# Performance work log

Hardware: AMD Instinct MI355X
Metric: run time of the kernel (lower is better)

## Reference

```python
import jax, jax.numpy as jnp
import numpy as np

# dims
B, N, M, R = 2, 16384, 512, 8      # batch, points, modes (slices), register tokens
D = 384                             # q_dim == kv_dim
H, DH = 8, 48                       # heads, dim_heads
P = 3                               # phys_dim
NF = DH // (2 * P)                  # rope freqs per physical axis (8)
FH = 1024                           # gated FFN hidden
L = 2                               # num_interleaved_layers
MINLF, MAXLF = -5.0, 3.0
EPS_LN = 1e-5
EPS_NORM = 1e-8


def _ln(x, g, b):
    m = jnp.mean(x, -1, keepdims=True)
    v = jnp.var(x, -1, keepdims=True)
    return (x - m) * jax.lax.rsqrt(v + EPS_LN) * g + b


def _rope_cs(coords):
    # coords: (B, S, P) -> cos/sin of shape (B, S, DH//2)
    freqs = jnp.exp(jnp.linspace(MINLF, MAXLF, NF))
    ang = (coords[..., :, None] * freqs).reshape(coords.shape[:-1] + (P * NF,))
    return jnp.cos(ang), jnp.sin(ang)


def _apply_rope(t, c, s):
    # t: (B, S, H, DH); c,s: (B, S, DH//2)
    tp = t.reshape(t.shape[:-1] + (DH // 2, 2))
    t0, t1 = tp[..., 0], tp[..., 1]
    c = c[:, :, None, :]
    s = s[:, :, None, :]
    r = jnp.stack([t0 * c - t1 * s, t0 * s + t1 * c], axis=-1)
    return r.reshape(t.shape)


def _mha(qin, kin, vin, xq, xk, wq, bq, wk, bk, wv, bv, wo, bo):
    Bq, Sq, _ = qin.shape
    Sk = kin.shape[1]
    q = (qin @ wq + bq).reshape(Bq, Sq, H, DH)
    k = (kin @ wk + bk).reshape(Bq, Sk, H, DH)
    v = (vin @ wv + bv).reshape(Bq, Sk, H, DH)
    cq, sq = _rope_cs(xq)
    ck, sk = _rope_cs(xk)
    q = _apply_rope(q, cq, sq)
    k = _apply_rope(k, ck, sk)
    scores = jnp.einsum('bqhd,bkhd->bhqk', q, k) / np.sqrt(DH).astype(np.float32)
    a = jax.nn.softmax(scores, axis=-1)
    o = jnp.einsum('bhqk,bkhd->bqhd', a, v).reshape(Bq, Sq, H * DH)
    return o @ wo + bo


def _subgen(feat, w, b):
    # Transolver slice generator: softmax over modes per point; mass == 1.
    tf = jax.nn.softmax(feat @ w + b, axis=-1)          # (B, S, M) trial_func
    tt = jnp.swapaxes(tf, 1, 2)                          # (B, M, S) trial_in_t
    inv = 1.0 / (jnp.sum(tf, axis=1) + EPS_NORM)         # (B, M) inv_trial_norm
    return tf, tt, inv[..., None]


def setup_inputs() -> dict:
    key = jax.random.key(0)
    ks = iter(jax.random.split(key, 64))
    nrm = lambda shape: jax.random.normal(next(ks), shape, dtype=jnp.float32)
    w = lambda shape: nrm(shape) * 0.02
    inp = {}
    inp['qx'] = nrm((B, N, D))
    inp['kvx'] = nrm((B, N, D))
    inp['x'] = jax.random.uniform(next(ks), (B, N, P), dtype=jnp.float32)
    inp['reg_tok_qx'] = nrm((B, R, D))
    inp['reg_tok_x'] = jax.random.uniform(next(ks), (B, R, P), dtype=jnp.float32)
    inp['subq_w'] = w((D, M)); inp['subq_b'] = jnp.zeros((M,))
    inp['subkv_w'] = w((D, M)); inp['subkv_b'] = jnp.zeros((M,))
    inp['nq_g'] = jnp.ones((D,)); inp['nq_b'] = jnp.zeros((D,))
    inp['nkv_g'] = jnp.ones((D,)); inp['nkv_b'] = jnp.zeros((D,))
    inp['a0_wq'] = w((D, H * DH)); inp['a0_bq'] = jnp.zeros((H * DH,))
    inp['a0_wk'] = w((D, H * DH)); inp['a0_bk'] = jnp.zeros((H * DH,))
    inp['a0_wv'] = w((D, H * DH)); inp['a0_bv'] = jnp.zeros((H * DH,))
    inp['a0_wo'] = w((H * DH, D)); inp['a0_bo'] = jnp.zeros((D,))
    inp['out_g'] = jnp.ones((D,)); inp['out_b'] = jnp.zeros((D,))
    inp['L_wq'] = w((L, D, H * DH)); inp['L_bq'] = jnp.zeros((L, H * DH))
    inp['L_wk'] = w((L, D, H * DH)); inp['L_bk'] = jnp.zeros((L, H * DH))
    inp['L_wv'] = w((L, D, H * DH)); inp['L_bv'] = jnp.zeros((L, H * DH))
    inp['L_wo'] = w((L, H * DH, D)); inp['L_bo'] = jnp.zeros((L, D))
    inp['L_ang'] = jnp.ones((L, D)); inp['L_anb'] = jnp.zeros((L, D))
    inp['L_fng'] = jnp.ones((L, D)); inp['L_fnb'] = jnp.zeros((L, D))
    inp['L_wg'] = w((L, D, FH)); inp['L_bg'] = jnp.zeros((L, FH))
    inp['L_wu'] = w((L, D, FH)); inp['L_bu'] = jnp.zeros((L, FH))
    inp['L_wd'] = w((L, FH, D)); inp['L_bd'] = jnp.zeros((L, D))
    return inp


def reference(qx, kvx, x, reg_tok_qx, reg_tok_x,
              subq_w, subq_b, subkv_w, subkv_b,
              nq_g, nq_b, nkv_g, nkv_b,
              a0_wq, a0_bq, a0_wk, a0_bk, a0_wv, a0_bv, a0_wo, a0_bo,
              out_g, out_b,
              L_wq, L_bq, L_wk, L_bk, L_wv, L_bv, L_wo, L_bo,
              L_ang, L_anb, L_fng, L_fnb,
              L_wg, L_bg, L_wu, L_bu, L_wd, L_bd):
    tfq, ttq, invq = _subgen(qx, subq_w, subq_b)
    _, ttkv, invkv = _subgen(kvx, subkv_w, subkv_b)
    qx_proj = jnp.matmul(ttq, qx) * invq          # (B, M, D)
    kvx_proj = jnp.matmul(ttkv, kvx) * invkv      # (B, M, D)
    xq_proj = jnp.matmul(ttq, x) * invq           # (B, M, P)
    xk_proj = jnp.matmul(ttkv, x) * invkv         # (B, M, P)
    q_full = jnp.concatenate([qx_proj, reg_tok_qx], axis=1)   # (B, M+R, D)
    xq_full = jnp.concatenate([xq_proj, reg_tok_x], axis=1)   # (B, M+R, P)
    q = _ln(q_full, nq_g, nq_b)
    kv = _ln(kvx_proj, nkv_g, nkv_b)
    y = _mha(q, kv, kv, xq_full, xk_proj,
             a0_wq, a0_bq, a0_wk, a0_bk, a0_wv, a0_bv, a0_wo, a0_bo) + q_full
    for i in range(L):
        h = _ln(y, L_fng[i], L_fnb[i])
        h = (jax.nn.silu(h @ L_wg[i] + L_bg[i]) * (h @ L_wu[i] + L_bu[i])) @ L_wd[i] + L_bd[i]
        y = h + y
        qn = _ln(y, L_ang[i], L_anb[i])
        y = _mha(qn, kv, kv, xq_full, xk_proj,
                 L_wq[i], L_bq[i], L_wk[i], L_bk[i], L_wv[i], L_bv[i], L_wo[i], L_bo[i]) + y
    y = _ln(y, out_g, out_b)
    y_proj = y[:, :M, :]
    reg_token = y[:, M:, :]
    y_recon = jnp.matmul(tfq, y_proj)             # (B, N, D)
    return (y_recon, reg_token)
```

## Files before the change

kernel.cpp:

```cpp
#include <hip/hip_runtime.h>


typedef __attribute__((ext_vector_type(8))) short short8;
typedef __attribute__((ext_vector_type(4))) float floatx4;

__device__ __forceinline__ float b2f(short s) {
    unsigned u = ((unsigned)(unsigned short)s) << 16;
    return __builtin_bit_cast(float, u);
}
__device__ __forceinline__ short f2b(float f) {
    unsigned u = __builtin_bit_cast(unsigned, f);
    unsigned r = (u + 0x7fffu + ((u >> 16) & 1u)) >> 16;
    return (short)r;
}

__device__ __forceinline__ void gload_lds16(const short* g, short* l) {
    __builtin_amdgcn_global_load_lds(
        (const __attribute__((address_space(1))) void*)(g),
        (__attribute__((address_space(3))) void*)(l), 16, 0, 0);
}

__global__ __launch_bounds__(256) void cvt_bf16_2(
    const float* __restrict__ srcA, const float* __restrict__ srcB,
    short* __restrict__ dstA, short* __restrict__ dstB, long n)
{
    const float* src = blockIdx.y ? srcB : srcA;
    short* dst = blockIdx.y ? dstB : dstA;
    long i = ((long)blockIdx.x * 256 + threadIdx.x) * 4;
    if (i + 4 <= n) {
        float4 v = *(const float4*)(src + i);
        short o[4] = {f2b(v.x), f2b(v.y), f2b(v.z), f2b(v.w)};
        *(short4*)(dst + i) = *(short4*)o;
    } else {
        for (long j = i; j < n; j++) dst[j] = f2b(src[j]);
    }
}

template <int EPI, bool SPLITK>
__global__ __launch_bounds__(256) void gemm_nt(
    const short* __restrict__ A, int lda, long sAb, long sAh,
    const short* __restrict__ Bm, int ldb, long sBb, long sBh,
    void* Cp, int ldc, long sCb, long sCh,
    const float* __restrict__ bias, int biasRow, int bzs,
    const float* aux, int ldaux,
    int Mrows, int Ncols, int Kdim, int nb, int KC)
{
    int z = blockIdx.z;
    int b = z % nb;
    int rest = z / nb;
    long aoff = (long)b * sAb, boff = (long)b * sBb;
    long coff = (long)b * sCb + (long)rest * sCh;
    int k_begin = 0, kEnd = Kdim;
    if (SPLITK) {
        k_begin = rest * KC;
        int ke = k_begin + KC;
        kEnd = ke < Kdim ? ke : Kdim;
    } else {
        aoff += (long)rest * sAh;
        boff += (long)rest * sBh;
    }
    if (bias) bias += (long)rest * bzs;
    const short* Ap = A + aoff;
    const short* Bp = Bm + boff;

    int row0 = blockIdx.x * 128, col0 = blockIdx.y * 128;
    __shared__ __align__(16) short As[3 * 128 * 32];
    __shared__ __align__(16) short Bs[3 * 128 * 32];
    int tid = threadIdx.x, lane = tid & 63, wv = tid >> 6;
    int wr = (wv >> 1) * 64, wc = (wv & 1) * 64;
    int lr = lane & 15, lq = lane >> 4;

    const bool fullMN = (row0 + 128 <= Mrows) && (col0 + 128 <= Ncols);
    const int kLen = kEnd - k_begin;
    const int nSteps = (kLen + 31) >> 5;
    const bool useRing = fullMN && ((kLen & 31) == 0);

    const int frow = (wv << 5) + (lane >> 2);
    const int fk = (lane & 3) << 3;
    const short* gA0 = Ap + (long)(row0 + frow) * lda + fk;
    const short* gA1 = gA0 + 16 * (long)lda;
    const short* gB0 = Bp + (long)(col0 + frow) * ldb + fk;
    const short* gB1 = gB0 + 16 * (long)ldb;
    short* lA0 = As + (wv << 10);
    short* lA1 = lA0 + 512;
    short* lB0 = Bs + (wv << 10);
    short* lB1 = lB0 + 512;

    auto stageFast = [&](int slot, int k0) {
        int bo = slot << 12;
        gload_lds16(gA0 + k0, lA0 + bo);
        gload_lds16(gA1 + k0, lA1 + bo);
        gload_lds16(gB0 + k0, lB0 + bo);
        gload_lds16(gB1 + k0, lB1 + bo);
    };
    auto stageAny = [&](int slot, int k0) {
        if (fullMN && (k0 + 32 <= kEnd)) {
            stageFast(slot, k0);
        } else {
            short* Ab = As + (slot << 12);
            short* Bb = Bs + (slot << 12);
#pragma unroll
            for (int io = 0; io < 2; io++) {
                int sid = tid * 2 + io;
                int r = sid >> 2, sg = sid & 3;
                int gk = k0 + sg * 8;
                short8 va, vb;
#pragma unroll
                for (int j = 0; j < 8; j++) { va[j] = 0; vb[j] = 0; }
                int gra = row0 + r, grb = col0 + r;
                if (gra < Mrows) {
                    const short* p = Ap + (long)gra * lda + gk;
                    if (gk + 8 <= kEnd) va = *(const short8*)p;
                    else { for (int j = 0; j < 8; j++) if (gk + j < kEnd) va[j] = p[j]; }
                }
                if (grb < Ncols) {
                    const short* p = Bp + (long)grb * ldb + gk;
                    if (gk + 8 <= kEnd) vb = *(const short8*)p;
                    else { for (int j = 0; j < 8; j++) if (gk + j < kEnd) vb[j] = p[j]; }
                }
                *(short8*)&Ab[r * 32 + sg * 8] = va;
                *(short8*)&Bb[r * 32 + sg * 8] = vb;
            }
        }
    };

    floatx4 acc[4][4];
#pragma unroll
    for (int i = 0; i < 4; i++)
#pragma unroll
        for (int j = 0; j < 4; j++)
#pragma unroll
            for (int e = 0; e < 4; e++) acc[i][j][e] = 0.f;

    auto compute = [&](int slot) {
        const int co = slot << 12;
        short8 af[4], bfv[4];
#pragma unroll
        for (int mt = 0; mt < 4; mt++)
            af[mt] = *(const short8*)&As[co + (wr + mt * 16 + lr) * 32 + lq * 8];
#pragma unroll
        for (int nt = 0; nt < 4; nt++)
            bfv[nt] = *(const short8*)&Bs[co + (wc + nt * 16 + lr) * 32 + lq * 8];
#pragma unroll
        for (int mt = 0; mt < 4; mt++)
#pragma unroll
            for (int nt = 0; nt < 4; nt++)
                acc[mt][nt] = __builtin_amdgcn_mfma_f32_16x16x32_bf16(
                    af[mt], bfv[nt], acc[mt][nt], 0, 0, 0);
    };

    if (useRing) {
        stageFast(0, k_begin);
        if (nSteps > 1) stageFast(1, k_begin + 32);
        int slotCur = 0, slotPre = 2;
        for (int s = 0; s < nSteps; s++) {
            if (s < nSteps - 1)
                asm volatile("s_waitcnt vmcnt(4)" ::: "memory");
            else
                asm volatile("s_waitcnt vmcnt(0)" ::: "memory");
            __builtin_amdgcn_s_barrier();
            __builtin_amdgcn_sched_barrier(0);
            if (s + 2 < nSteps) stageFast(slotPre, k_begin + (s + 2) * 32);
            compute(slotCur);
            slotCur = (slotCur == 2) ? 0 : slotCur + 1;
            slotPre = (slotPre == 2) ? 0 : slotPre + 1;
        }
    } else {
        stageAny(0, k_begin);
        __syncthreads();
        for (int s = 0; s < nSteps; s++) {
            const int cur = s & 1;
            if (s + 1 < nSteps) stageAny(cur ^ 1, k_begin + (s + 1) * 32);
            compute(cur);
            __syncthreads();
        }
    }

    if (EPI == 5) {
        const float ropeScale = __builtin_bit_cast(float, KC);
        const float* cosT = aux;
        const float* sinT = aux + ldaux;
#pragma unroll
        for (int mt = 0; mt < 4; mt++) {
#pragma unroll
            for (int nt = 0; nt < 4; nt++) {
                int gcol = col0 + wc + nt * 16 + lr;
#pragma unroll
                for (int r = 0; r < 4; r++) {
                    int grow = row0 + wr + mt * 16 + lq * 4 + r;
                    float v = acc[mt][nt][r] + bias[gcol];
                    float partner = __shfl_xor(v, 1, 64);
                    if (fullMN || (grow < Mrows && gcol < Ncols)) {
                        int pi = (gcol >> 1) % 24;
                        float cc = cosT[(long)grow * 24 + pi];
                        float ss = sinT[(long)grow * 24 + pi];
                        float o = (gcol & 1) ? (partner * ss + v * cc)
                                             : (v * cc - partner * ss);
                        ((short*)Cp)[coff + (long)grow * ldc + gcol] =
                            f2b(o * ropeScale);
                    }
                }
            }
        }
    } else if (EPI == 6) {
#pragma unroll
        for (int mt = 0; mt < 4; mt++) {
#pragma unroll
            for (int nt = 0; nt < 4; nt++) {
                int gcol = col0 + wc + nt * 16 + lr;
#pragma unroll
                for (int r = 0; r < 4; r++) {
                    int grow = row0 + wr + mt * 16 + lq * 4 + r;
                    float v = acc[mt][nt][r] + bias[gcol];
                    float partner = __shfl_xor(v, 1, 64);
                    if (((gcol & 1) == 0) && (fullMN || grow < Mrows)) {
                        float s = v / (1.f + __expf(-v));
                        ((short*)Cp)[coff + (long)grow * ldc + (gcol >> 1)] =
                            f2b(s * partner);
                    }
                }
            }
        }
    } else if (fullMN) {
#pragma unroll
        for (int mt = 0; mt < 4; mt++) {
#pragma unroll
            for (int nt = 0; nt < 4; nt++) {
                int gcol = col0 + wc + nt * 16 + lr;
#pragma unroll
                for (int r = 0; r < 4; r++) {
                    int grow = row0 + wr + mt * 16 + lq * 4 + r;
                    float v = acc[mt][nt][r];
                    if (bias) v += bias[biasRow ? grow : gcol];
                    long idx = coff + (long)grow * ldc + gcol;
                    if (EPI == 0) {
                        ((float*)Cp)[idx] = v;
                    } else if (EPI == 1) {
                        ((short*)Cp)[idx] = f2b(v);
                    } else {
                        float rr = aux[(long)grow * ldaux + gcol];
                        ((float*)Cp)[idx] = v + rr;
                    }
                }
            }
        }
    } else {
#pragma unroll
        for (int mt = 0; mt < 4; mt++) {
#pragma unroll
            for (int nt = 0; nt < 4; nt++) {
                int gcol = col0 + wc + nt * 16 + lr;
#pragma unroll
                for (int r = 0; r < 4; r++) {
                    int grow = row0 + wr + mt * 16 + lq * 4 + r;
                    if (grow < Mrows && gcol < Ncols) {
                        float v = acc[mt][nt][r];
                        if (bias) v += bias[biasRow ? grow : gcol];
                        long idx = coff + (long)grow * ldc + gcol;
                        if (EPI == 0) {
                            ((float*)Cp)[idx] = v;
                        } else if (EPI == 1) {
                            ((short*)Cp)[idx] = f2b(v);
                        } else {
                            float rr = aux[(long)grow * ldaux + gcol];
                            ((float*)Cp)[idx] = v + rr;
                        }
                    }
                }
            }
        }
    }
}

__global__ __launch_bounds__(64) void attn_fused(
    const short* __restrict__ Q, const short* __restrict__ K,
    const short* __restrict__ V, short* __restrict__ O)
{
    int tile = blockIdx.x;
    int b = blockIdx.y, h = blockIdx.z;
    int lane = threadIdx.x;
    int lr = lane & 15, lq = lane >> 4;
    int q0 = tile * 16;

    const short* Qb = Q + (long)b * 199680 + h * 48;
    const short* Kb = K + (long)b * 196608 + h * 48;
    const short* Vb = V + (long)b * 196608 + (long)h * 48 * 512;
    short* Ob = O + (long)b * 199680 + h * 48;

    __shared__ __align__(16) short Plds[16 * 512];
    char* pb = (char*)Plds;

    short8 aq0, aq1;
    {
        int qr = q0 + lr; if (qr > 519) qr = 519;
        const short* qp = Qb + (long)qr * 384;
        aq0 = *(const short8*)(qp + lq * 8);
        short8 z;
#pragma unroll
        for (int j = 0; j < 8; j++) z[j] = 0;
        aq1 = (lq < 2) ? *(const short8*)(qp + 32 + lq * 8) : z;
    }

    floatx4 s[32];
#pragma unroll
    for (int nt = 0; nt < 32; nt++)
#pragma unroll
        for (int e = 0; e < 4; e++) s[nt][e] = 0.f;
#pragma unroll
    for (int nt = 0; nt < 32; nt++) {
        const short* kp = Kb + (long)(nt * 16 + lr) * 384;
        short8 b0 = *(const short8*)(kp + lq * 8);
        short8 b1 = *(const short8*)(kp + 32 + lq * 8);
        s[nt] = __builtin_amdgcn_mfma_f32_16x16x32_bf16(aq0, b0, s[nt], 0, 0, 0);
        s[nt] = __builtin_amdgcn_mfma_f32_16x16x32_bf16(aq1, b1, s[nt], 0, 0, 0);
    }

    float mx[4], sum[4], inv[4];
#pragma unroll
    for (int r = 0; r < 4; r++) mx[r] = -1e30f;
#pragma unroll
    for (int nt = 0; nt < 32; nt++)
#pragma unroll
        for (int r = 0; r < 4; r++) mx[r] = fmaxf(mx[r], s[nt][r]);
#pragma unroll
    for (int o = 8; o; o >>= 1)
#pragma unroll
        for (int r = 0; r < 4; r++) mx[r] = fmaxf(mx[r], __shfl_xor(mx[r], o, 64));
#pragma unroll
    for (int r = 0; r < 4; r++) sum[r] = 0.f;
#pragma unroll
    for (int nt = 0; nt < 32; nt++)
#pragma unroll
        for (int r = 0; r < 4; r++) {
            float e = __expf(s[nt][r] - mx[r]);
            s[nt][r] = e;
            sum[r] += e;
        }
#pragma unroll
    for (int o = 8; o; o >>= 1)
#pragma unroll
        for (int r = 0; r < 4; r++) sum[r] += __shfl_xor(sum[r], o, 64);
#pragma unroll
    for (int r = 0; r < 4; r++) inv[r] = 1.0f / sum[r];

#pragma unroll
    for (int nt = 0; nt < 32; nt++)
#pragma unroll
        for (int r = 0; r < 4; r++) {
            int row = lq * 4 + r, col = nt * 16 + lr;
            int byo = ((row * 512 + col) * 2) ^ ((row & 7) << 4);
            *(short*)(pb + byo) = f2b(s[nt][r] * inv[r]);
        }

    floatx4 o2[3];
#pragma unroll
    for (int nt = 0; nt < 3; nt++)
#pragma unroll
        for (int e = 0; e < 4; e++) o2[nt][e] = 0.f;
#pragma unroll
    for (int ks = 0; ks < 16; ks++) {
        int byo = ((lr * 512 + ks * 32 + lq * 8) * 2) ^ ((lr & 7) << 4);
        short8 ap = *(const short8*)(pb + byo);
#pragma unroll
        for (int nt = 0; nt < 3; nt++) {
            short8 bv = *(const short8*)(Vb + (long)(nt * 16 + lr) * 512 +
                                         ks * 32 + lq * 8);
            o2[nt] = __builtin_amdgcn_mfma_f32_16x16x32_bf16(ap, bv, o2[nt], 0, 0, 0);
        }
    }
#pragma unroll
    for (int nt = 0; nt < 3; nt++)
#pragma unroll
        for (int r = 0; r < 4; r++) {
            int q = q0 + lq * 4 + r;
            if (q < 520)
                Ob[(long)q * 384 + nt * 16 + lr] = f2b(o2[nt][r]);
        }
}

__global__ __launch_bounds__(256) void softmax_rows(
    const short* __restrict__ src, short* __restrict__ dstN,
    short* __restrict__ dstT, int rowsPerBatch)
{
    int n0 = blockIdx.x * 32;
    __shared__ __align__(16) short tile[32 * 512];
    int tid = threadIdx.x;
    const short8* gsrc = (const short8*)(src + (long)n0 * 512);
    short8* t8 = (short8*)tile;
#pragma unroll
    for (int i = 0; i < 8; i++) t8[tid + i * 256] = gsrc[tid + i * 256];
    __syncthreads();
    int wv = tid >> 6, lane = tid & 63;
#pragma unroll
    for (int rr = 0; rr < 8; rr++) {
        int r = wv * 8 + rr;
        short8 s = *(const short8*)&tile[r * 512 + lane * 8];
        float v[8];
        float mx = -1e30f;
#pragma unroll
        for (int j = 0; j < 8; j++) { v[j] = b2f(s[j]); mx = fmaxf(mx, v[j]); }
#pragma unroll
        for (int o = 32; o; o >>= 1) mx = fmaxf(mx, __shfl_xor(mx, o, 64));
        float sum = 0.f;
#pragma unroll
        for (int j = 0; j < 8; j++) { v[j] = __expf(v[j] - mx); sum += v[j]; }
#pragma unroll
        for (int o = 32; o; o >>= 1) sum += __shfl_xor(sum, o, 64);
        float inv = 1.0f / sum;
        short8 o8;
#pragma unroll
        for (int j = 0; j < 8; j++) o8[j] = f2b(v[j] * inv);
        *(short8*)&tile[r * 512 + lane * 8] = o8;
        if (dstN) *(short8*)(dstN + (long)(n0 + r) * 512 + lane * 8) = o8;
    }
    if (!dstT) return;
    __syncthreads();
    int b = n0 / rowsPerBatch;
    int nn0 = n0 % rowsPerBatch;
#pragma unroll
    for (int rep = 0; rep < 2; rep++) {
        int m = tid + rep * 256;
        short tmp[32];
#pragma unroll
        for (int i = 0; i < 32; i++) tmp[i] = tile[i * 512 + m];
        short* dst = dstT + ((long)b * 512 + m) * rowsPerBatch + nn0;
#pragma unroll
        for (int i = 0; i < 4; i++) *(short8*)(dst + i * 8) = *(const short8*)&tmp[i * 8];
    }
}

__global__ __launch_bounds__(256) void build_augT(
    const short* __restrict__ src, const float* __restrict__ xin,
    short* __restrict__ augT)
{
    int n0 = blockIdx.x * 32, jb = blockIdx.y, b = blockIdx.z;
    int t = threadIdx.x;
    if (jb == 12) {
        if (t < 128) {
            int jj = t >> 5, i = t & 31;
            float val = (jj < 3) ? xin[((long)b * 16384 + n0 + i) * 3 + jj] : 1.0f;
            augT[((long)(b * 512 + 384 + jj)) * 16384 + n0 + i] = f2b(val);
        }
        return;
    }
    __shared__ short tl[32][33];
    int j0 = jb * 32;
#pragma unroll
    for (int rep = 0; rep < 4; rep++) {
        int sid = t + rep * 256;
        int i = sid >> 5, j = sid & 31;
        tl[i][j] = src[((long)b * 16384 + n0 + i) * 384 + j0 + j];
    }
    __syncthreads();
#pragma unroll
    for (int rep = 0; rep < 4; rep++) {
        int sid = t + rep * 256;
        int j = sid >> 5, i = sid & 31;
        augT[((long)(b * 512 + j0 + j)) * 16384 + n0 + i] = tl[i][j];
    }
}

template <bool ISQ>
__global__ __launch_bounds__(256) void prep_kernel(
    const float* __restrict__ parts, const float* __restrict__ regqx,
    const float* __restrict__ regx, const float* __restrict__ gam,
    const float* __restrict__ bet, float* __restrict__ qfull,
    short* __restrict__ lnout, float* __restrict__ cb, float* __restrict__ sb,
    int Srows)
{
    int m = blockIdx.x, b = blockIdx.y, t = threadIdx.x;
    __shared__ float sh[388];
    __shared__ float r1[256], r2[256];
    bool isReg = ISQ && (m >= 512);
    if (isReg) {
        int rr = m - 512;
        for (int c = t; c < 384; c += 256) sh[c] = regqx[((long)b * 8 + rr) * 384 + c];
        if (t < 3) sh[384 + t] = regx[((long)b * 8 + rr) * 3 + t];
    } else {
        for (int c = t; c < 388; c += 256) {
            float s = 0.f;
#pragma unroll
            for (int sp = 0; sp < 16; sp++)
                s += parts[(((long)(sp * 2 + b)) * 512 + m) * 512 + c];
            sh[c] = s;
        }
    }
    __syncthreads();
    float inv = isReg ? 1.0f : 1.0f / (sh[387] + 1e-8f);
    float ls = 0.f, lq = 0.f;
    for (int c = t; c < 384; c += 256) {
        float v = sh[c] * inv;
        ls += v; lq += v * v;
    }
    r1[t] = ls; r2[t] = lq;
    __syncthreads();
    for (int o = 128; o; o >>= 1) {
        if (t < o) { r1[t] += r1[t + o]; r2[t] += r2[t + o]; }
        __syncthreads();
    }
    float mean = r1[0] * (1.f / 384.f);
    float var = r2[0] * (1.f / 384.f) - mean * mean;
    float rs = rsqrtf(var + 1e-5f);
    long row = (long)b * Srows + m;
    for (int c = t; c < 384; c += 256) {
        float v = sh[c] * inv;
        if (ISQ) qfull[row * 384 + c] = v;
        lnout[row * 384 + c] = f2b((v - mean) * rs * gam[c] + bet[c]);
    }
    if (t < 24) {
        int p = t >> 3, f = t & 7;
        float coord = sh[384 + p] * inv;
        float ang = coord * __expf(-5.0f + (float)f * (8.0f / 7.0f));
        cb[row * 24 + t] = cosf(ang);
        sb[row * 24 + t] = sinf(ang);
    }
}

struct TEntry { const float* src; short* dst; int rows, cols, cs, co; };
struct TTable { TEntry e[20]; int cnt; };

__global__ __launch_bounds__(256) void transpose_many(
    TTable tab, const float* __restrict__ a0bk, const float* __restrict__ Lbk,
    const float* __restrict__ a0bv, const float* __restrict__ Lbv,
    const float* __restrict__ Lbg, const float* __restrict__ Lbu,
    float* __restrict__ bkAll, float* __restrict__ bvAll,
    float* __restrict__ bgu)
{
    int id = blockIdx.z;
    int t = threadIdx.x;
    if (id >= tab.cnt) {
        if (blockIdx.x == 0 && blockIdx.y == 0) {
            for (int i = t; i < 1152; i += 256) {
                int l = i / 384, j = i % 384;
                bkAll[i] = l ? Lbk[(l - 1) * 384 + j] : a0bk[j];
                bvAll[i] = l ? Lbv[(l - 1) * 384 + j] : a0bv[j];
            }
            for (int i = t; i < 4096; i += 256) {
                int l = i >> 11, j = i & 2047;
                bgu[i] = (j & 1) ? Lbu[l * 1024 + (j >> 1)]
                                 : Lbg[l * 1024 + (j >> 1)];
            }
        }
        return;
    }
    TEntry E = tab.e[id];
    int r0 = blockIdx.y * 32, c0 = blockIdx.x * 32;
    if (r0 >= E.rows || c0 >= E.cols) return;
    __shared__ short tl[32][33];
#pragma unroll
    for (int rep = 0; rep < 4; rep++) {
        int sid = t + rep * 256;
        int i = sid >> 5, j = sid & 31;
        int r = r0 + i, c = c0 + j;
        tl[i][j] = (r < E.rows && c < E.cols) ? f2b(E.src[(long)r * E.cols + c])
                                              : (short)0;
    }
    __syncthreads();
#pragma unroll
    for (int rep = 0; rep < 4; rep++) {
        int sid = t + rep * 256;
        int j = sid >> 5, i = sid & 31;
        int c = c0 + j, r = r0 + i;
        if (c < E.cols && r < E.rows)
            E.dst[((long)c * E.cs + E.co) * E.rows + r] = tl[i][j];
    }
}

__global__ __launch_bounds__(256) void ln_kernel(
    const float* __restrict__ in, const float* __restrict__ gam,
    const float* __restrict__ bet, short* __restrict__ out)
{
    long row = blockIdx.x;
    int t = threadIdx.x;
    const float* xr = in + row * 384;
    float v0 = xr[t];
    float v1 = (t < 128) ? xr[t + 256] : 0.f;
    __shared__ float r1[256], r2[256];
    r1[t] = v0 + v1; r2[t] = v0 * v0 + v1 * v1;
    __syncthreads();
    for (int o = 128; o; o >>= 1) {
        if (t < o) { r1[t] += r1[t + o]; r2[t] += r2[t + o]; }
        __syncthreads();
    }
    float mean = r1[0] * (1.f / 384.f);
    float var = r2[0] * (1.f / 384.f) - mean * mean;
    float rs = rsqrtf(var + 1e-5f);
    out[row * 384 + t] = f2b((v0 - mean) * rs * gam[t] + bet[t]);
    if (t < 128)
        out[row * 384 + t + 256] =
            f2b((v1 - mean) * rs * gam[t + 256] + bet[t + 256]);
}

__global__ __launch_bounds__(256) void outln_kernel(
    const float* __restrict__ in, const float* __restrict__ gam,
    const float* __restrict__ bet, short* __restrict__ yln,
    short* __restrict__ ylnT, float* __restrict__ regout)
{
    int m = blockIdx.x, b = blockIdx.y, t = threadIdx.x;
    long row = (long)b * 520 + m;
    const float* xr = in + row * 384;
    float v0 = xr[t];
    float v1 = (t < 128) ? xr[t + 256] : 0.f;
    __shared__ float r1[256], r2[256];
    r1[t] = v0 + v1; r2[t] = v0 * v0 + v1 * v1;
    __syncthreads();
    for (int o = 128; o; o >>= 1) {
        if (t < o) { r1[t] += r1[t + o]; r2[t] += r2[t + o]; }
        __syncthreads();
    }
    float mean = r1[0] * (1.f / 384.f);
    float var = r2[0] * (1.f / 384.f) - mean * mean;
    float rs = rsqrtf(var + 1e-5f);
    float o0 = (v0 - mean) * rs * gam[t] + bet[t];
    float o1 = (t < 128) ? (v1 - mean) * rs * gam[t + 256] + bet[t + 256] : 0.f;
    if (m < 512) {
        short s0 = f2b(o0);
        yln[((long)b * 512 + m) * 384 + t] = s0;
        ylnT[((long)b * 384 + t) * 512 + m] = s0;
        if (t < 128) {
            short s1 = f2b(o1);
            yln[((long)b * 512 + m) * 384 + t + 256] = s1;
            ylnT[((long)b * 384 + t + 256) * 512 + m] = s1;
        }
    } else {
        float* dst = regout + ((long)b * 8 + (m - 512)) * 384;
        dst[t] = o0;
        if (t < 128) dst[t + 256] = o1;
    }
}

__device__ __forceinline__ int chk3(float v, float lo, float hi) {
    if (!(v == v) || fabsf(v) > 3e38f) return 1;
    if (v < lo || v > hi) return 2;
    return 0;
}

__global__ __launch_bounds__(256) void probe_stages(
    const float* __restrict__ nqg, const float* __restrict__ qx,
    const short* __restrict__ subqT, const short* __restrict__ tfq,
    const float* __restrict__ qfull, const short* __restrict__ qln,
    const short* __restrict__ kvln, const float* __restrict__ cq,
    const short* __restrict__ Kr, const short* __restrict__ Vt,
    const short* __restrict__ Oc, const short* __restrict__ hg,
    const float* __restrict__ y, const short* __restrict__ ylnT,
    const float* __restrict__ dout, int* __restrict__ diag)
{
    int t = threadIdx.x;
    int task = blockIdx.x;
    __shared__ int sNaN, sRange, sPl;
    if (t == 0) { sNaN = 0; sRange = 0; sPl = 0; }
    __syncthreads();

    auto scanB = [&](const short* p, long n, float lo, float hi) {
        long stride = n / 2048; if (stride < 1) stride = 1;
        for (int j = 0; j < 8; j++) {
            long i = ((long)(t * 8 + j)) * stride;
            if (i >= n) break;
            int c = chk3(b2f(p[i]), lo, hi);
            if (c == 1) atomicOr(&sNaN, 1);
            else if (c == 2) atomicOr(&sRange, 1);
        }
    };
    auto scanF = [&](const float* p, long n, float lo, float hi) {
        long stride = n / 2048; if (stride < 1) stride = 1;
        for (int j = 0; j < 8; j++) {
            long i = ((long)(t * 8 + j)) * stride;
            if (i >= n) break;
            int c = chk3(p[i], lo, hi);
            if (c == 1) atomicOr(&sNaN, 1);
            else if (c == 2) atomicOr(&sRange, 1);
        }
    };

    int res = 0;
    if (task == 0) {
        int d1;
        {
            bool f32ones = true;
            for (int i = 0; i < 8; i++) if (nqg[i] != 1.0f) f32ones = false;
            d1 = f32ones ? 0 : 1;
        }
        int d2;
        {
            int plaus = 0;
            for (int i = 0; i < 64; i++) {
                float v = qx[i];
                float a = fabsf(v);
                if (v == v && a > 1e-4f && a < 16.f) plaus++;
            }
            d2 = (plaus >= 56) ? 0 : 1;
        }
        if (t == 0) diag[2] = d1 * 3 + d2;
        return;
    } else if (task == 1) {
        long n = 196608L;
        long stride = n / 2048; if (stride < 1) stride = 1;
        for (int j = 0; j < 8; j++) {
            long i = ((long)(t * 8 + j)) * stride;
            if (i >= n) break;
            float v = b2f(subqT[i]);
            float a = fabsf(v);
            if (!(v == v)) atomicOr(&sNaN, 1);
            else if (a >= 1e-7f && a <= 2.f) atomicAdd(&sPl, 1);
        }
        __syncthreads();
        res = sNaN ? 1 : ((sPl < 1228) ? 2 : 0);
        if (t == 0) diag[2 + 1] = res;
        return;
    }
    switch (task) {
        case 2: scanB(tfq, 16777216L, -1e-4f, 1.0001f); break;
        case 3: scanF(qfull, 399360L, -1e3f, 1e3f); break;
        case 4: scanB(qln, 399360L, -100.f, 100.f); break;
        case 5: scanB(kvln, 393216L, -100.f, 100.f); break;
        case 6: scanF(cq, 24960L, -1.0001f, 1.0001f); break;
        case 7: scanB(Kr, 399360L, -1e3f, 1e3f); break;
        case 8: scanB(Vt, 1179648L, -1e3f, 1e3f); break;
        case 9: scanB(Oc, 399360L, -1e3f, 1e3f); break;
        case 10: scanB(hg, 1064960L, -1e4f, 1e4f); break;
        case 11: scanF(y, 399360L, -1e5f, 1e5f); break;
        case 12: scanB(ylnT, 393216L, -100.f, 100.f); break;
        case 13: scanF(dout, 12589056L, -1e3f, 1e3f); break;
        default: break;
    }
    __syncthreads();
    res = sNaN ? 1 : (sRange ? 2 : 0);
    if (t == 0) diag[2 + task] = res;
}

__global__ void probe_combine(int* __restrict__ diag, unsigned wsMB)
{
    int firstBad = 0, kind = 0;
    for (int idx = 1; idx <= 13; idx++) {
        int r = diag[2 + idx];
        if (r != 0 && firstBad == 0) { firstBad = idx; kind = (r == 2) ? 1 : 0; }
    }
    int dd = diag[2];
    int wb;
    if (wsMB < 32) wb = 0; else if (wsMB < 48) wb = 1;
    else if (wsMB < 64) wb = 2; else if (wsMB < 80) wb = 3;
    else if (wsMB < 96) wb = 4; else if (wsMB < 100) wb = 5;
    else if (wsMB < 112) wb = 6; else if (wsMB < 128) wb = 7;
    else if (wsMB < 160) wb = 8; else if (wsMB < 224) wb = 9;
    else if (wsMB < 512) wb = 10; else wb = 11;

    int code = firstBad + 14 * (kind + 2 * (wb + 12 * dd));
    diag[0] = code;
    diag[1] = (firstBad == 0 && dd == 0) ? 1 : 0;
}

__global__ __launch_bounds__(256) void fill_out(float* __restrict__ out,
                                                const int* __restrict__ diag,
                                                long n)
{
    if (diag[1]) return;
    int code = diag[0];
    long i0 = ((long)blockIdx.x * 256 + threadIdx.x) * 8;
#pragma unroll
    for (int j = 0; j < 8; j++)
        if (i0 + j < n) out[i0 + j] = 0.f;
    if (i0 == 0)
        out[1] = ldexpf(1.0f + (float)(code & 255) * (1.0f / 256.0f),
                        (code >> 8) + 14);
}

#define LAUNCH_GEMM(EPI, SPLIT, GX, GY, GZ, A, LDA, SAB, SAH, B_, LDB, SBB,   \
                    SBH, C_, LDC, SCB, SCH, BIAS, BROW, BZS, AUX, LDAUX, M_,  \
                    N_, K_, NB, KC)                                           \
    gemm_nt<EPI, SPLIT><<<dim3(GX, GY, GZ), 256, 0, stream>>>(                \
        (const short*)(A), LDA, SAB, SAH, (const short*)(B_), LDB, SBB, SBH,  \
        (void*)(C_), LDC, SCB, SCH, (const float*)(BIAS), BROW, BZS,          \
        (const float*)(AUX), LDAUX, M_, N_, K_, NB, KC)

extern "C" void kernel_launch(void* const* d_in, const int* in_sizes, int n_in,
                              void* d_out, int out_size, void* d_ws,
                              size_t ws_size, hipStream_t stream)
{
    (void)in_sizes; (void)n_in; (void)out_size;
    const float* qx    = (const float*)d_in[0];
    const float* kvx   = (const float*)d_in[1];
    const float* xin   = (const float*)d_in[2];
    const float* regqx = (const float*)d_in[3];
    const float* regx  = (const float*)d_in[4];
    const float* subq_b  = (const float*)d_in[6];
    const float* subkv_b = (const float*)d_in[8];
    const float* nq_g = (const float*)d_in[9];
    const float* nq_b = (const float*)d_in[10];
    const float* nkv_g = (const float*)d_in[11];
    const float* nkv_b = (const float*)d_in[12];
    const float* a0_bq = (const float*)d_in[14];
    const float* a0_bk = (const float*)d_in[16];
    const float* a0_bv = (const float*)d_in[18];
    const float* a0_bo = (const float*)d_in[20];
    const float* out_g = (const float*)d_in[21];
    const float* out_b = (const float*)d_in[22];
    const float* L_bq = (const float*)d_in[24];
    const float* L_bk = (const float*)d_in[26];
    const float* L_bv = (const float*)d_in[28];
    const float* L_bo = (const float*)d_in[30];
    const float* L_ang = (const float*)d_in[31];
    const float* L_anb = (const float*)d_in[32];
    const float* L_fng = (const float*)d_in[33];
    const float* L_fnb = (const float*)d_in[34];
    const float* L_bg = (const float*)d_in[36];
    const float* L_bu = (const float*)d_in[38];
    const float* L_bd = (const float*)d_in[40];

    char* W = (char*)d_ws;
    short* qxb   = (short*)(W + 0L);
    short* kvxb  = (short*)(W + 25165824L);
    short* tfT   = (short*)(W + 50331648L);
    short* tfq   = (short*)(W + 83886080L);
    short* aug   = (short*)(W + 117440512L);
    short* Wt    = (short*)(W + 167772160L);
    float* qfull = (float*)(W + 176816128L);
    short* qln   = (short*)(W + 178413568L);
    short* kvln  = (short*)(W + 179212288L);
    float* cq    = (float*)(W + 179998720L);
    float* sq    = (float*)(W + 180098560L);
    float* ck    = (float*)(W + 180198400L);
    float* sk    = (float*)(W + 180296704L);
    float* y     = (float*)(W + 180395008L);
    short* hln   = (short*)(W + 181992448L);
    short* ylnT  = (short*)(W + 182791168L);
    short* VtAll = (short*)(W + 209136640L);
    short* Oc    = (short*)(W + 213396480L);
    float* bkAll = (float*)(W + 214195200L);
    float* bvAll = (float*)(W + 214200320L);
    float* bgu   = (float*)(W + 214205440L);
    short* Qr    = (short*)(W + 215792640L);
    short* hg    = (short*)(W + 218164224L);
    int*   diag  = (int*)(W + 220294144L);
    float* parts = (float*)(W + 220298240L);
    short* KrAll = tfT;

    short* subqT  = Wt + 0L;
    short* subkvT = Wt + 196608L;
    auto QW  = [&](int l) { return Wt + 393216L  + (long)l * 147456L; };
    auto KW  = [&](int l) { return Wt + 835584L  + (long)l * 147456L; };
    auto VW  = [&](int l) { return Wt + 1277952L + (long)l * 147456L; };
    auto OW  = [&](int l) { return Wt + 1720320L + (long)l * 147456L; };
    auto GUW = [&](int l) { return Wt + 2162688L + (long)l * 786432L; };
    auto DW  = [&](int l) { return Wt + 3735552L + (long)l * 393216L; };

    auto fbits = [](float f) {
        union { float f; int i; } u; u.f = f; return u.i;
    };

    cvt_bf16_2<<<dim3(12288, 2), 256, 0, stream>>>(qx, kvx, qxb, kvxb,
                                                   12582912L);

    TTable tt;
    int ti = 0;
    auto addT = [&](const void* s, short* dst, int r, int c, int cs, int co) {
        tt.e[ti].src = (const float*)s; tt.e[ti].dst = dst;
        tt.e[ti].rows = r; tt.e[ti].cols = c;
        tt.e[ti].cs = cs; tt.e[ti].co = co; ti++;
    };
    addT(d_in[5], subqT, 384, 512, 1, 0);
    addT(d_in[7], subkvT, 384, 512, 1, 0);
    addT(d_in[13], QW(0), 384, 384, 1, 0);
    addT(d_in[15], KW(0), 384, 384, 1, 0);
    addT(d_in[17], VW(0), 384, 384, 1, 0);
    addT(d_in[19], OW(0), 384, 384, 1, 0);
    for (int l = 0; l < 2; l++) {
        addT((const float*)d_in[23] + (long)l * 147456, QW(l + 1), 384, 384, 1, 0);
        addT((const float*)d_in[25] + (long)l * 147456, KW(l + 1), 384, 384, 1, 0);
        addT((const float*)d_in[27] + (long)l * 147456, VW(l + 1), 384, 384, 1, 0);
        addT((const float*)d_in[29] + (long)l * 147456, OW(l + 1), 384, 384, 1, 0);
        addT((const float*)d_in[35] + (long)l * 393216, GUW(l), 384, 1024, 2, 0);
        addT((const float*)d_in[37] + (long)l * 393216, GUW(l), 384, 1024, 2, 1);
        addT((const float*)d_in[39] + (long)l * 393216, DW(l), 1024, 384, 1, 0);
    }
    tt.cnt = ti;
    transpose_many<<<dim3(32, 32, 21), 256, 0, stream>>>(
        tt, a0_bk, L_bk, a0_bv, L_bv, L_bg, L_bu, bkAll, bvAll, bgu);

    LAUNCH_GEMM(1, false, 256, 4, 1, qxb, 384, 0L, 0L, subqT, 384, 0L, 0L,
                aug, 512, 0L, 0L, subq_b, 0, 0, nullptr, 0, 32768, 512, 384, 1, 0);
    softmax_rows<<<1024, 256, 0, stream>>>(aug, tfq, tfT, 16384);
    build_augT<<<dim3(512, 13, 2), 256, 0, stream>>>(qxb, xin, aug);
    LAUNCH_GEMM(0, true, 4, 4, 32, tfT, 16384, 8388608L, 0L, aug, 16384,
                8388608L, 0L, parts, 512, 262144L, 524288L, nullptr, 0, 0,
                nullptr, 0, 512, 512, 16384, 2, 1024);
    prep_kernel<true><<<dim3(520, 2), 256, 0, stream>>>(
        parts, regqx, regx, nq_g, nq_b, qfull, qln, cq, sq, 520);

    LAUNCH_GEMM(1, false, 256, 4, 1, kvxb, 384, 0L, 0L, subkvT, 384, 0L, 0L,
                aug, 512, 0L, 0L, subkv_b, 0, 0, nullptr, 0, 32768, 512, 384, 1, 0);
    softmax_rows<<<1024, 256, 0, stream>>>(aug, nullptr, tfT, 16384);
    build_augT<<<dim3(512, 13, 2), 256, 0, stream>>>(kvxb, xin, aug);
    LAUNCH_GEMM(0, true, 4, 4, 32, tfT, 16384, 8388608L, 0L, aug, 16384,
                8388608L, 0L, parts, 512, 262144L, 524288L, nullptr, 0, 0,
                nullptr, 0, 512, 512, 16384, 2, 1024);
    prep_kernel<false><<<dim3(512, 2), 256, 0, stream>>>(
        parts, nullptr, nullptr, nkv_g, nkv_b, nullptr, kvln, ck, sk, 512);

    const float qscale = 0.14433756729740643f;
    LAUNCH_GEMM(5, false, 8, 3, 3, kvln, 384, 0L, 0L, KW(0), 384, 0L, 147456L,
                KrAll, 384, 0L, 393216L, bkAll, 0, 384, ck, 24576,
                1024, 384, 384, 1, fbits(1.0f));
    LAUNCH_GEMM(1, false, 3, 4, 6, VW(0), 384, 0L, 147456L, kvln, 384,
                196608L, 0L, VtAll, 512, 196608L, 393216L, bvAll, 1, 384,
                nullptr, 0, 384, 512, 384, 2, 0);

    auto runMHA = [&](const short* qin, const short* wqT, const float* bq,
                      const short* woT, const float* bo, const float* res,
                      int lay) {
        LAUNCH_GEMM(5, false, 9, 3, 1, qin, 384, 0L, 0L, wqT, 384, 0L, 0L,
                    Qr, 384, 0L, 0L, bq, 0, 0, cq, 24960,
                    1040, 384, 384, 1, fbits(qscale));
        attn_fused<<<dim3(33, 2, 8), 64, 0, stream>>>(
            Qr, KrAll + (long)lay * 393216L, VtAll + (long)lay * 393216L, Oc);
        LAUNCH_GEMM(3, false, 9, 3, 1, Oc, 384, 0L, 0L, woT, 384, 0L, 0L,
                    y, 384, 0L, 0L, bo, 0, 0, res, 384, 1040, 384, 384, 1, 0);
    };

    runMHA(qln, QW(0), a0_bq, OW(0), a0_bo, qfull, 0);

    for (int l = 0; l < 2; l++) {
        ln_kernel<<<1040, 256, 0, stream>>>(y, L_fng + l * 384, L_fnb + l * 384, hln);
        LAUNCH_GEMM(6, false, 9, 16, 1, hln, 384, 0L, 0L, GUW(l), 384, 0L, 0L,
                    hg, 1024, 0L, 0L, bgu + l * 2048, 0, 0, nullptr, 0,
                    1040, 2048, 384, 1, 0);
        LAUNCH_GEMM(3, false, 9, 3, 1, hg, 1024, 0L, 0L, DW(l), 1024, 0L, 0L,
                    y, 384, 0L, 0L, L_bd + l * 384, 0, 0, y, 384,
                    1040, 384, 1024, 1, 0);
        ln_kernel<<<1040, 256, 0, stream>>>(y, L_ang + l * 384, L_anb + l * 384, hln);
        runMHA(hln, QW(l + 1), L_bq + l * 384, OW(l + 1), L_bo + l * 384, y,
               l + 1);
    }

    short* yln = hln;
    float* regout = (float*)d_out + 12582912L;
    outln_kernel<<<dim3(520, 2), 256, 0, stream>>>(y, out_g, out_b, yln, ylnT,
                                                   regout);
    LAUNCH_GEMM(0, false, 128, 3, 2, tfq, 512, 8388608L, 0L, ylnT, 512,
                196608L, 0L, (float*)d_out, 384, 6291456L, 0L, nullptr, 0, 0,
                nullptr, 0, 16384, 384, 512, 2, 0);

    probe_stages<<<14, 256, 0, stream>>>(
        nq_g, qx, subqT, tfq, qfull, qln, kvln, cq, KrAll, VtAll, Oc, hg, y,
        ylnT, (const float*)d_out, diag);
    probe_combine<<<1, 1, 0, stream>>>(diag, (unsigned)(ws_size >> 20));
    fill_out<<<6147, 256, 0, stream>>>((float*)d_out, diag, 12589056L);
}
```

Before: 1.043 ms.

## Split fused attention into score GEMM, row softmax, and PV GEMM

Replaces the single-wave fused attention kernel with three launches: a batched GEMM writing fp32 scores to a workspace buffer, a row-wise softmax kernel producing bf16 probabilities, and a batched GEMM multiplying by V. The aim is to reuse the tiled, LDS-staged GEMM path instead of a 64-thread kernel that loads K and V straight from global memory, which is poorly occupied. The cost is an extra round trip through global memory for the score and probability matrices, plus two more kernel launches per attention call.

```diff
diff --git a/kernel.cpp b/kernel.cpp
--- a/kernel.cpp
+++ b/kernel.cpp
@@ -272,112 +272,6 @@
     }
 }
 
-__global__ __launch_bounds__(64) void attn_fused(
-    const short* __restrict__ Q, const short* __restrict__ K,
-    const short* __restrict__ V, short* __restrict__ O)
-{
-    int tile = blockIdx.x;
-    int b = blockIdx.y, h = blockIdx.z;
-    int lane = threadIdx.x;
-    int lr = lane & 15, lq = lane >> 4;
-    int q0 = tile * 16;
-
-    const short* Qb = Q + (long)b * 199680 + h * 48;
-    const short* Kb = K + (long)b * 196608 + h * 48;
-    const short* Vb = V + (long)b * 196608 + (long)h * 48 * 512;
-    short* Ob = O + (long)b * 199680 + h * 48;
-
-    __shared__ __align__(16) short Plds[16 * 512];
-    char* pb = (char*)Plds;
-
-    short8 aq0, aq1;
-    {
-        int qr = q0 + lr; if (qr > 519) qr = 519;
-        const short* qp = Qb + (long)qr * 384;
-        aq0 = *(const short8*)(qp + lq * 8);
-        short8 z;
-#pragma unroll
-        for (int j = 0; j < 8; j++) z[j] = 0;
-        aq1 = (lq < 2) ? *(const short8*)(qp + 32 + lq * 8) : z;
-    }
-
-    floatx4 s[32];
-#pragma unroll
-    for (int nt = 0; nt < 32; nt++)
-#pragma unroll
-        for (int e = 0; e < 4; e++) s[nt][e] = 0.f;
-#pragma unroll
-    for (int nt = 0; nt < 32; nt++) {
-        const short* kp = Kb + (long)(nt * 16 + lr) * 384;
-        short8 b0 = *(const short8*)(kp + lq * 8);
-        short8 b1 = *(const short8*)(kp + 32 + lq * 8);
-        s[nt] = __builtin_amdgcn_mfma_f32_16x16x32_bf16(aq0, b0, s[nt], 0, 0, 0);
-        s[nt] = __builtin_amdgcn_mfma_f32_16x16x32_bf16(aq1, b1, s[nt], 0, 0, 0);
-    }
-
-    float mx[4], sum[4], inv[4];
-#pragma unroll
-    for (int r = 0; r < 4; r++) mx[r] = -1e30f;
-#pragma unroll
-    for (int nt = 0; nt < 32; nt++)
-#pragma unroll
-        for (int r = 0; r < 4; r++) mx[r] = fmaxf(mx[r], s[nt][r]);
-#pragma unroll
-    for (int o = 8; o; o >>= 1)
-#pragma unroll
-        for (int r = 0; r < 4; r++) mx[r] = fmaxf(mx[r], __shfl_xor(mx[r], o, 64));
-#pragma unroll
-    for (int r = 0; r < 4; r++) sum[r] = 0.f;
-#pragma unroll
-    for (int nt = 0; nt < 32; nt++)
-#pragma unroll
-        for (int r = 0; r < 4; r++) {
-            float e = __expf(s[nt][r] - mx[r]);
-            s[nt][r] = e;
-            sum[r] += e;
-        }
-#pragma unroll
-    for (int o = 8; o; o >>= 1)
-#pragma unroll
-        for (int r = 0; r < 4; r++) sum[r] += __shfl_xor(sum[r], o, 64);
-#pragma unroll
-    for (int r = 0; r < 4; r++) inv[r] = 1.0f / sum[r];
-
-#pragma unroll
-    for (int nt = 0; nt < 32; nt++)
-#pragma unroll
-        for (int r = 0; r < 4; r++) {
-            int row = lq * 4 + r, col = nt * 16 + lr;
-            int byo = ((row * 512 + col) * 2) ^ ((row & 7) << 4);
-            *(short*)(pb + byo) = f2b(s[nt][r] * inv[r]);
-        }
-
-    floatx4 o2[3];
-#pragma unroll
-    for (int nt = 0; nt < 3; nt++)
-#pragma unroll
-        for (int e = 0; e < 4; e++) o2[nt][e] = 0.f;
-#pragma unroll
-    for (int ks = 0; ks < 16; ks++) {
-        int byo = ((lr * 512 + ks * 32 + lq * 8) * 2) ^ ((lr & 7) << 4);
-        short8 ap = *(const short8*)(pb + byo);
-#pragma unroll
-        for (int nt = 0; nt < 3; nt++) {
-            short8 bv = *(const short8*)(Vb + (long)(nt * 16 + lr) * 512 +
-                                         ks * 32 + lq * 8);
-            o2[nt] = __builtin_amdgcn_mfma_f32_16x16x32_bf16(ap, bv, o2[nt], 0, 0, 0);
-        }
-    }
-#pragma unroll
-    for (int nt = 0; nt < 3; nt++)
-#pragma unroll
-        for (int r = 0; r < 4; r++) {
-            int q = q0 + lq * 4 + r;
-            if (q < 520)
-                Ob[(long)q * 384 + nt * 16 + lr] = f2b(o2[nt][r]);
-        }
-}
-
 __global__ __launch_bounds__(256) void softmax_rows(
     const short* __restrict__ src, short* __restrict__ dstN,
     short* __restrict__ dstT, int rowsPerBatch)
@@ -564,6 +458,30 @@
         if (c < E.cols && r < E.rows)
             E.dst[((long)c * E.cs + E.co) * E.rows + r] = tl[i][j];
     }
+}
+
+__global__ __launch_bounds__(256) void attn_softmax(
+    const float* __restrict__ Sc, short* __restrict__ P)
+{
+    int row = blockIdx.x * 4 + (threadIdx.x >> 6);
+    int lane = threadIdx.x & 63;
+    const float* sr = Sc + (long)row * 512 + lane * 8;
+    float v[8];
+    float mx = -1e30f;
+#pragma unroll
+    for (int j = 0; j < 8; j++) { v[j] = sr[j]; mx = fmaxf(mx, v[j]); }
+#pragma unroll
+    for (int o = 32; o; o >>= 1) mx = fmaxf(mx, __shfl_xor(mx, o, 64));
+    float sum = 0.f;
+#pragma unroll
+    for (int j = 0; j < 8; j++) { v[j] = __expf(v[j] - mx); sum += v[j]; }
+#pragma unroll
+    for (int o = 32; o; o >>= 1) sum += __shfl_xor(sum, o, 64);
+    float inv = 1.0f / sum;
+    short8 o8;
+#pragma unroll
+    for (int j = 0; j < 8; j++) o8[j] = f2b(v[j] * inv);
+    *(short8*)(P + (long)row * 512 + lane * 8) = o8;
 }
 
 __global__ __launch_bounds__(256) void ln_kernel(
@@ -823,6 +741,8 @@
     float* y     = (float*)(W + 180395008L);
     short* hln   = (short*)(W + 181992448L);
     short* ylnT  = (short*)(W + 182791168L);
+    float* Sc    = (float*)(W + 183577600L);
+    short* Pm    = (short*)(W + 200616960L);
     short* VtAll = (short*)(W + 209136640L);
     short* Oc    = (short*)(W + 213396480L);
     float* bkAll = (float*)(W + 214195200L);
@@ -910,8 +830,15 @@
         LAUNCH_GEMM(5, false, 9, 3, 1, qin, 384, 0L, 0L, wqT, 384, 0L, 0L,
                     Qr, 384, 0L, 0L, bq, 0, 0, cq, 24960,
                     1040, 384, 384, 1, fbits(qscale));
-        attn_fused<<<dim3(33, 2, 8), 64, 0, stream>>>(
-            Qr, KrAll + (long)lay * 393216L, VtAll + (long)lay * 393216L, Oc);
+        LAUNCH_GEMM(0, false, 5, 4, 16, Qr, 384, 199680L, 48L,
+                    KrAll + (long)lay * 393216L, 384, 196608L, 48L,
+                    Sc, 512, 2129920L, 266240L, nullptr, 0, 0, nullptr, 0,
+                    520, 512, 48, 2, 0);
+        attn_softmax<<<2080, 256, 0, stream>>>(Sc, Pm);
+        LAUNCH_GEMM(1, false, 5, 1, 16, Pm, 512, 2129920L, 266240L,
+                    VtAll + (long)lay * 393216L, 512, 196608L, 24576L,
+                    Oc, 384, 199680L, 48L, nullptr, 0, 0, nullptr, 0,
+                    520, 48, 512, 2, 0);
         LAUNCH_GEMM(3, false, 9, 3, 1, Oc, 384, 0L, 0L, woT, 384, 0L, 0L,
                     y, 384, 0L, 0L, bo, 0, 0, res, 384, 1040, 384, 384, 1, 0);
     };
```

New measurement: 975.7 us. 6.5% less time.
